# Kernel optimization log

Measured on AMD Instinct MI355X. Metric: run time of the kernel, lower is better.

Reference implementation:

```python
import jax, jax.numpy as jnp
import numpy as np

NOPEN = 64
NNIN = 16
NUM_OUTPUT = 64
NLAYER = 4
H = 0.1
TF = 1.0
N_NODES = 50000
N_EDGES = 1600000


def setup_inputs() -> dict:
    key = jax.random.key(0)
    k1, k2, k3, k4, k5, k6 = jax.random.split(key, 6)
    xn = jax.random.normal(k1, (1, NNIN, N_NODES), dtype=jnp.float32)
    iInd = jax.random.randint(k2, (N_EDGES,), 0, N_NODES)
    jInd = jax.random.randint(k3, (N_EDGES,), 0, N_NODES)
    # learned parameters per original init
    K1Nopen = jax.random.normal(k4, (NOPEN, NNIN), dtype=jnp.float32) * 0.01
    KN1 = jnp.eye(NOPEN, dtype=jnp.float32) + jax.random.uniform(k5, (NOPEN, NOPEN), dtype=jnp.float32) * 0.001
    KNclose = jax.random.normal(k6, (NUM_OUTPUT, NOPEN), dtype=jnp.float32) * 0.01
    return {"xn": xn, "iInd": iInd, "jInd": jInd, "n_nodes": N_NODES,
            "K1Nopen": K1Nopen, "KN1": KN1, "KNclose": KNclose}


def _gcn_norm(I, J, n_nodes, dtype):
    # add self-loops, symmetric normalization deg^{-1/2}[row]*deg^{-1/2}[col]
    loops = jnp.arange(n_nodes, dtype=I.dtype)
    I2 = jnp.concatenate([I, loops])
    J2 = jnp.concatenate([J, loops])
    ew = jnp.ones(I2.shape[0], dtype=dtype)
    deg = jax.ops.segment_sum(ew, J2, num_segments=n_nodes)
    dinv = jnp.where(deg > 0, 1.0 / jnp.sqrt(deg), 0.0)
    w = dinv[I2] * dinv[J2]
    return I2, J2, w


def reference(xn, iInd, jInd, n_nodes, K1Nopen, KN1, KNclose):
    I, J, w = _gcn_norm(iInd, jInd, n_nodes, xn.dtype)  # [E+N]

    # OpenFlatLayer: 1x1 conv1d with K1Nopen + relu (openclose=True, norm=False)
    x = jax.nn.relu(jnp.einsum('oi,bin->bon', K1Nopen, xn))  # [1, nopen, N]

    dt = TF / NLAYER
    wb = w[None, None, :]
    for _ in range(NLAYER):
        # nodeGrad: edge features [1, nopen, E]
        g = wb * (x[:, :, I] - x[:, :, J])
        # singleLayer (openclose=False): conv(K), relu, conv(K.t())
        z = jax.nn.relu(jnp.einsum('oi,bie->boe', KN1, g))
        z = jnp.einsum('io,bie->boe', KN1, z)
        # edgeDiv: scatter-add w*z at I minus at J
        wz = jnp.moveaxis(wb * z, -1, 0)  # [E, 1, nopen]
        div = (jax.ops.segment_sum(wz, I, num_segments=n_nodes)
               - jax.ops.segment_sum(wz, J, num_segments=n_nodes))
        div = jnp.moveaxis(div, 0, -1)  # [1, nopen, N]
        # forward Euler: step layer returns -h*div, integrated with dt
        x = x - dt * H * div

    # CloseLayer: 1x1 conv1d, squeeze().t(), log_softmax over channels
    xc = jnp.einsum('oi,bin->bon', KNclose, x)[0].T  # [N, num_output]
    return jax.nn.log_softmax(xc, axis=1)
```

## Files before the change

### kernel.cpp

```cpp
#include <hip/hip_runtime.h>

#define NN 50000
#define NE 1600000
#define C 64
#define NIN 16
#define DTH 0.025f
#define ASC 16.0f
#define USC 64.0f
#define SDIV 16384.0f
#define SLOT 128

#define NB2 256
#define NPB 196
#define CAP 16384
#define ABLK 1024
#define EPB 1563
#define RND 2048
#define BINC 32

typedef _Float16 f16x2 __attribute__((ext_vector_type(2)));
typedef float f32x2 __attribute__((ext_vector_type(2)));
union U32H2 { uint32_t u; f16x2 h; };

__global__ void k_setup(const float* __restrict__ KN1, const float* __restrict__ KNc,
                        const float* __restrict__ K1,
                        float* __restrict__ KN1T, float* __restrict__ KNcT,
                        float* __restrict__ K1T, float* __restrict__ M2s,
                        float* __restrict__ KMs, int* __restrict__ gcur) {
    if (threadIdx.x < NB2) gcur[threadIdx.x] = 0;
    for (int idx = threadIdx.x; idx < C * C; idx += blockDim.x) {
        int o = idx >> 6, i = idx & 63;
        KN1T[i * C + o] = KN1[o * C + i];
        KNcT[i * C + o] = KNc[o * C + i];
    }
    for (int idx = threadIdx.x; idx < C * NIN; idx += blockDim.x) {
        int o = idx >> 4, i = idx & 15;
        K1T[i * C + o] = K1[o * NIN + i];
    }
    for (int idx = threadIdx.x; idx < C * C; idx += blockDim.x) {
        int p = idx >> 6, o = idx & 63;
        float s1 = 0.f, s2 = 0.f;
        for (int i = 0; i < C; i++) {
            s1 = fmaf(KN1[o * C + i], KN1[p * C + i], s1);
            s2 = fmaf(KNc[o * C + i], KN1[p * C + i], s2);
        }
        M2s[idx] = s1;
        KMs[idx] = s2;
    }
}

__launch_bounds__(256)
__global__ void k_binA(const int* __restrict__ iInd, const int* __restrict__ jInd,
                       int* __restrict__ gcur, uint32_t* __restrict__ stg) {
    __shared__ uint32_t bins[NB2][BINC];
    __shared__ int bcnt[NB2];
    __shared__ int gbase[NB2];
    int tid = threadIdx.x;
    int eBeg = blockIdx.x * EPB;
    int eEnd = eBeg + EPB; if (eEnd > NE) eEnd = NE;
    for (int rb = eBeg; rb < eEnd; rb += RND) {
        for (int b = tid; b < NB2; b += 256) bcnt[b] = 0;
        __syncthreads();
        int rEnd = rb + RND; if (rEnd > eEnd) rEnd = eEnd;
        for (int e = rb + tid; e < rEnd; e += 256) {
            int i = __builtin_nontemporal_load(&iInd[e]);
            int j = __builtin_nontemporal_load(&jInd[e]);
            {
                int b = (unsigned)i / NPB;
                uint32_t ent = ((unsigned)(i - b * NPB) << 17) | (unsigned)j;
                int pos = atomicAdd(&bcnt[b], 1);
                if (pos < BINC) bins[b][pos] = ent;
                else { int gp = atomicAdd(&gcur[b], 1);
                       if (gp < CAP) stg[(size_t)b * CAP + gp] = ent; }
            }
            {
                int b = (unsigned)j / NPB;
                uint32_t ent = ((unsigned)(j - b * NPB) << 17) | 0x10000u | (unsigned)i;
                int pos = atomicAdd(&bcnt[b], 1);
                if (pos < BINC) bins[b][pos] = ent;
                else { int gp = atomicAdd(&gcur[b], 1);
                       if (gp < CAP) stg[(size_t)b * CAP + gp] = ent; }
            }
        }
        __syncthreads();
        {
            int c = bcnt[tid]; if (c > BINC) c = BINC;
            gbase[tid] = (c > 0) ? atomicAdd(&gcur[tid], c) : 0;
        }
        __syncthreads();
        for (int idx = tid; idx < NB2 * BINC; idx += 256) {
            int b = idx >> 5, k = idx & (BINC - 1);
            int c = bcnt[b]; if (c > BINC) c = BINC;
            if (k < c) {
                int pos = gbase[b] + k;
                if (pos < CAP) stg[(size_t)b * CAP + pos] = bins[b][k];
            }
        }
        __syncthreads();
    }
}

__launch_bounds__(1024)
__global__ void k_binB(const int* __restrict__ gcur, const uint32_t* __restrict__ stg,
                       unsigned* __restrict__ pk, float* __restrict__ dinv,
                       uint32_t* __restrict__ adjp) {
    __shared__ unsigned lcnt[NPB];
    int b = blockIdx.x, tid = threadIdx.x;
    if (tid < NPB) lcnt[tid] = 0;
    __syncthreads();
    int cnt = gcur[b]; if (cnt > CAP) cnt = CAP;
    int n0 = b * NPB;
    for (int k = tid; k < cnt; k += 1024) {
        uint32_t ent = stg[(size_t)b * CAP + k];
        int tl = (int)(ent >> 17);
        unsigned sign = (ent >> 16) & 1u;
        unsigned other = ent & 0xFFFFu;
        unsigned ret = atomicAdd(&lcnt[tl], 1u + (sign << 16));
        unsigned slot = ret & 0xFFFFu;
        if (slot < SLOT) adjp[(((unsigned)(n0 + tl)) << 7) + slot] = other | (sign << 31);
    }
    __syncthreads();
    if (tid < NPB) {
        int n = n0 + tid;
        if (n < NN) {
            unsigned v = lcnt[tid];
            unsigned c = v & 0xFFFFu; if (c > SLOT) c = SLOT;
            unsigned deg = (v >> 16) + 1u;
            pk[n] = (deg << 16) | c;
            dinv[n] = 1.0f / sqrtf((float)deg);
        }
    }
}

__global__ void k_weight(const unsigned* __restrict__ pk, const float* __restrict__ dinv,
                         uint32_t* __restrict__ adjp) {
    int idx = blockIdx.x * 256 + threadIdx.x;
    int n = idx >> 7, p = idx & (SLOT - 1);
    int cnt = (int)(pk[n] & 0xFFFFu); if (cnt > SLOT) cnt = SLOT;
    int pad = (cnt + 31) & ~31;
    if (p < cnt) {
        uint32_t e = adjp[idx];
        int other = (int)(e & 0xFFFFu);
        float a = ASC * dinv[n] * dinv[other];
        float w = 0.5f * a * a;
        if (e >> 31) w = -w;
        U32H2 t; t.u = (unsigned)other; t.h.y = (_Float16)w;
        adjp[idx] = t.u;
    } else if (p < pad) {
        adjp[idx] = 0u;
    }
}

static __device__ __forceinline__ void store_u8(uint32_t* __restrict__ u8, int n, int lane, float su) {
    float v1 = __shfl_down(su, 1, 64);
    float v2 = __shfl_down(su, 2, 64);
    float v3 = __shfl_down(su, 3, 64);
    if ((lane & 3) == 0) {
        int p0 = __builtin_amdgcn_cvt_pk_fp8_f32(su, v1, 0, false);
        int p1 = __builtin_amdgcn_cvt_pk_fp8_f32(v2, v3, p0, true);
        u8[n * 16 + (lane >> 2)] = (uint32_t)p1;
    }
}

__launch_bounds__(256)
__global__ void k_open_u(const float* __restrict__ xn, const float* __restrict__ K1T,
                         const float* __restrict__ KN1T, const float* __restrict__ KNcT,
                         _Float16* __restrict__ u0, uint32_t* __restrict__ u8,
                         float* __restrict__ co) {
    __shared__ float sK1T[NIN * C];
    __shared__ float sKT[C * C];
    __shared__ float sKc[C * C];
    for (int idx = threadIdx.x; idx < NIN * C; idx += 256) sK1T[idx] = K1T[idx];
    for (int idx = threadIdx.x; idx < C * C; idx += 256) { sKT[idx] = KN1T[idx]; sKc[idx] = KNcT[idx]; }
    __syncthreads();
    int wv = threadIdx.x >> 6, lane = threadIdx.x & 63;
    int n = blockIdx.x * 4 + wv;
    float acc = 0.f;
#pragma unroll
    for (int i = 0; i < NIN; i++)
        acc = fmaf(sK1T[i * C + lane], xn[i * NN + n], acc);
    float xr = fmaxf(acc, 0.f);
    float ua = 0.f, oc = 0.f;
    for (int i = 0; i < C; i++) {
        float xi = __shfl(xr, i, 64);
        ua = fmaf(sKT[i * C + lane], xi, ua);
        oc = fmaf(sKc[i * C + lane], xi, oc);
    }
    u0[(size_t)n * C + lane] = (_Float16)ua;
    store_u8(u8, n, lane, ua * USC);
    co[(size_t)n * C + lane] = oc;
}

#define ACCR(WW, QQ, A0, A1, A2, A3, U0, U1, U2, U3) {                        \
    U32H2 aw; aw.u = (WW);                                                    \
    float w_ = (float)aw.h.y;                                                 \
    f32x2 lo_ = __builtin_amdgcn_cvt_pk_f32_fp8((int)(QQ), false);            \
    f32x2 hi_ = __builtin_amdgcn_cvt_pk_f32_fp8((int)(QQ), true);             \
    float d0_ = (U0) - lo_.x, d1_ = (U1) - lo_.y;                             \
    float d2_ = (U2) - hi_.x, d3_ = (U3) - hi_.y;                             \
    A0 = fmaf(w_, __builtin_fabsf(d0_), fmaf(__builtin_fabsf(w_), d0_, A0));  \
    A1 = fmaf(w_, __builtin_fabsf(d1_), fmaf(__builtin_fabsf(w_), d1_, A1));  \
    A2 = fmaf(w_, __builtin_fabsf(d2_), fmaf(__builtin_fabsf(w_), d2_, A2));  \
    A3 = fmaf(w_, __builtin_fabsf(d3_), fmaf(__builtin_fabsf(w_), d3_, A3));  \
}

#define GATHER2_BODY(PKA, ADJP, U8R)                                          \
    uint32_t unqA = (U8R)[nA * 16 + li];                                      \
    uint32_t unqB = (U8R)[nB * 16 + li];                                      \
    f32x2 alo = __builtin_amdgcn_cvt_pk_f32_fp8((int)unqA, false);            \
    f32x2 ahi = __builtin_amdgcn_cvt_pk_f32_fp8((int)unqA, true);             \
    f32x2 blo = __builtin_amdgcn_cvt_pk_f32_fp8((int)unqB, false);            \
    f32x2 bhi = __builtin_amdgcn_cvt_pk_f32_fp8((int)unqB, true);             \
    float uA0 = alo.x, uA1 = alo.y, uA2 = ahi.x, uA3 = ahi.y;                 \
    float uB0 = blo.x, uB1 = blo.y, uB2 = bhi.x, uB3 = bhi.y;                 \
    uint2 pk2_ = *(const uint2*)&(PKA)[nA];                                   \
    int degA = (int)(pk2_.x & 0xFFFFu); if (degA > SLOT) degA = SLOT;         \
    int degB = (int)(pk2_.y & 0xFFFFu); if (degB > SLOT) degB = SLOT;         \
    int padA = (degA + 31) & ~31, padB = (degB + 31) & ~31;                   \
    int baseA = nA << 7, baseB = nB << 7;                                     \
    int maxPad = padA > padB ? padA : padB;                                   \
    float aA0 = 0.f, aA1 = 0.f, aA2 = 0.f, aA3 = 0.f;                         \
    float aB0 = 0.f, aB1 = 0.f, aB2 = 0.f, aB3 = 0.f;                         \
    for (int c0 = 0; c0 < maxPad; c0 += 32) {                                 \
        uint32_t wA[8], qA[8], wB[8], qB[8];                                  \
        bool dA = c0 < padA, dB = c0 < padB;                                  \
        if (dA) {                                                             \
            _Pragma("unroll")                                                 \
            for (int r = 0; r < 8; r++) wA[r] = (ADJP)[baseA + c0 + r * 4 + g]; \
        }                                                                     \
        if (dB) {                                                             \
            _Pragma("unroll")                                                 \
            for (int r = 0; r < 8; r++) wB[r] = (ADJP)[baseB + c0 + r * 4 + g]; \
        }                                                                     \
        if (dA) {                                                             \
            _Pragma("unroll")                                                 \
            for (int r = 0; r < 8; r++) qA[r] = (U8R)[(wA[r] & 0xFFFFu) * 16 + li]; \
        }                                                                     \
        if (dB) {                                                             \
            _Pragma("unroll")                                                 \
            for (int r = 0; r < 8; r++) qB[r] = (U8R)[(wB[r] & 0xFFFFu) * 16 + li]; \
        }                                                                     \
        if (dA) {                                                             \
            _Pragma("unroll")                                                 \
            for (int r = 0; r < 8; r++) ACCR(wA[r], qA[r], aA0, aA1, aA2, aA3, uA0, uA1, uA2, uA3) \
        }                                                                     \
        if (dB) {                                                             \
            _Pragma("unroll")                                                 \
            for (int r = 0; r < 8; r++) ACCR(wB[r], qB[r], aB0, aB1, aB2, aB3, uB0, uB1, uB2, uB3) \
        }                                                                     \
    }                                                                         \
    aA0 += __shfl_xor(aA0, 16, 64); aA0 += __shfl_xor(aA0, 32, 64);           \
    aA1 += __shfl_xor(aA1, 16, 64); aA1 += __shfl_xor(aA1, 32, 64);           \
    aA2 += __shfl_xor(aA2, 16, 64); aA2 += __shfl_xor(aA2, 32, 64);           \
    aA3 += __shfl_xor(aA3, 16, 64); aA3 += __shfl_xor(aA3, 32, 64);           \
    aB0 += __shfl_xor(aB0, 16, 64); aB0 += __shfl_xor(aB0, 32, 64);           \
    aB1 += __shfl_xor(aB1, 16, 64); aB1 += __shfl_xor(aB1, 32, 64);           \
    aB2 += __shfl_xor(aB2, 16, 64); aB2 += __shfl_xor(aB2, 32, 64);           \
    aB3 += __shfl_xor(aB3, 16, 64); aB3 += __shfl_xor(aB3, 32, 64);           \
    float rA0 = __shfl(aA0, lane >> 2, 64), rA1 = __shfl(aA1, lane >> 2, 64); \
    float rA2 = __shfl(aA2, lane >> 2, 64), rA3 = __shfl(aA3, lane >> 2, 64); \
    float rB0 = __shfl(aB0, lane >> 2, 64), rB1 = __shfl(aB1, lane >> 2, 64); \
    float rB2 = __shfl(aB2, lane >> 2, 64), rB3 = __shfl(aB3, lane >> 2, 64); \
    float sA_lane = (lane & 2) ? ((lane & 1) ? rA3 : rA2)                     \
                               : ((lane & 1) ? rA1 : rA0);                    \
    float sB_lane = (lane & 2) ? ((lane & 1) ? rB3 : rB2)                     \
                               : ((lane & 1) ? rB1 : rB0);

#define RL(x, l) __int_as_float(__builtin_amdgcn_readlane(__float_as_int(x), (l)))

#define STAGE_MT(SMT, SRC) {                                                  \
    for (int idx = threadIdx.x; idx < C * C; idx += 256) {                    \
        int p_ = idx >> 6, c_ = idx & 63;                                     \
        (SMT)[(c_ << 6) | (p_ ^ ((c_ & 7) << 2))] = (SRC)[idx];               \
    }                                                                         \
}

#define MATVEC2(SMT, SAV, SBV, DUA, DUB) {                                    \
    float mA0_ = 0.f, mA1_ = 0.f, mB0_ = 0.f, mB1_ = 0.f;                     \
    int mb_ = (lane << 6), lx_ = (lane & 7) << 2;                             \
    _Pragma("unroll")                                                         \
    for (int p0 = 0; p0 < 64; p0 += 4) {                                      \
        const float4 mv = *(const float4*)&(SMT)[mb_ + (p0 ^ lx_)];           \
        mA0_ = fmaf(mv.x, RL(SAV, p0 + 0), mA0_);                             \
        mA1_ = fmaf(mv.y, RL(SAV, p0 + 1), mA1_);                             \
        mA0_ = fmaf(mv.z, RL(SAV, p0 + 2), mA0_);                             \
        mA1_ = fmaf(mv.w, RL(SAV, p0 + 3), mA1_);                             \
        mB0_ = fmaf(mv.x, RL(SBV, p0 + 0), mB0_);                             \
        mB1_ = fmaf(mv.y, RL(SBV, p0 + 1), mB1_);                             \
        mB0_ = fmaf(mv.z, RL(SBV, p0 + 2), mB0_);                             \
        mB1_ = fmaf(mv.w, RL(SBV, p0 + 3), mB1_);                             \
    }                                                                         \
    DUA = mA0_ + mA1_; DUB = mB0_ + mB1_;                                     \
}

__launch_bounds__(256, 8)
__global__ void k_gather_upd(const unsigned* __restrict__ pk, const uint32_t* __restrict__ adjp,
                             const uint32_t* __restrict__ u8r, const _Float16* __restrict__ ucur,
                             const float* __restrict__ M2s, float* __restrict__ sacc,
                             _Float16* __restrict__ unext, uint32_t* __restrict__ u8w, int beta) {
    __shared__ float sMt[C * C];
    STAGE_MT(sMt, M2s)
    __syncthreads();
    int wv = threadIdx.x >> 6, lane = threadIdx.x & 63;
    int g = lane >> 4, li = lane & 15;
    int nA = (blockIdx.x * 4 + wv) * 2;
    int nB = nA + 1;
    GATHER2_BODY(pk, adjp, u8r)
    float duA, duB;
    MATVEC2(sMt, sA_lane, sB_lane, duA, duB)
    float unewA = (float)ucur[(size_t)nA * C + lane] - (DTH / SDIV) * duA;
    float unewB = (float)ucur[(size_t)nB * C + lane] - (DTH / SDIV) * duB;
    unext[(size_t)nA * C + lane] = (_Float16)unewA;
    unext[(size_t)nB * C + lane] = (_Float16)unewB;
    store_u8(u8w, nA, lane, unewA * USC);
    store_u8(u8w, nB, lane, unewB * USC);
    size_t ixA = (size_t)nA * C + lane, ixB = (size_t)nB * C + lane;
    sacc[ixA] = beta ? (sacc[ixA] + sA_lane) : sA_lane;
    sacc[ixB] = beta ? (sacc[ixB] + sB_lane) : sB_lane;
}

__launch_bounds__(256, 8)
__global__ void k_gather_close(const unsigned* __restrict__ pk, const uint32_t* __restrict__ adjp,
                               const uint32_t* __restrict__ u8r, const float* __restrict__ KMs,
                               const float* __restrict__ sacc, const float* __restrict__ co,
                               float* __restrict__ out) {
    __shared__ float sKMt[C * C];
    STAGE_MT(sKMt, KMs)
    __syncthreads();
    int wv = threadIdx.x >> 6, lane = threadIdx.x & 63;
    int g = lane >> 4, li = lane & 15;
    int nA = (blockIdx.x * 4 + wv) * 2;
    int nB = nA + 1;
    GATHER2_BODY(pk, adjp, u8r)
    float stotA = sA_lane + sacc[(size_t)nA * C + lane];
    float stotB = sB_lane + sacc[(size_t)nB * C + lane];
    float dxA, dxB;
    MATVEC2(sKMt, stotA, stotB, dxA, dxB)
    float oA = co[(size_t)nA * C + lane] - (DTH / SDIV) * dxA;
    float oB = co[(size_t)nB * C + lane] - (DTH / SDIV) * dxB;
    float mA = oA, mB = oB;
#pragma unroll
    for (int off2 = 32; off2; off2 >>= 1) {
        mA = fmaxf(mA, __shfl_xor(mA, off2, 64));
        mB = fmaxf(mB, __shfl_xor(mB, off2, 64));
    }
    float sumA = expf(oA - mA), sumB = expf(oB - mB);
#pragma unroll
    for (int off2 = 32; off2; off2 >>= 1) {
        sumA += __shfl_xor(sumA, off2, 64);
        sumB += __shfl_xor(sumB, off2, 64);
    }
    out[(size_t)nA * C + lane] = oA - mA - logf(sumA);
    out[(size_t)nB * C + lane] = oB - mB - logf(sumB);
}

extern "C" void kernel_launch(void* const* d_in, const int* in_sizes, int n_in,
                              void* d_out, int out_size, void* d_ws, size_t ws_size,
                              hipStream_t stream) {
    (void)in_sizes; (void)n_in; (void)out_size; (void)ws_size;
    const float* xn   = (const float*)d_in[0];
    const int* iInd   = (const int*)d_in[1];
    const int* jInd   = (const int*)d_in[2];
    const float* K1   = (const float*)d_in[4];
    const float* KN1  = (const float*)d_in[5];
    const float* KNc  = (const float*)d_in[6];
    float* out = (float*)d_out;

    char* base = (char*)d_ws;
    size_t off = 0;
    auto alloc = [&](size_t bytes) { char* p = base + off; off = (off + bytes + 255) & ~(size_t)255; return p; };
    float* KN1T = (float*)alloc(C * C * 4);
    float* KNcT = (float*)alloc(C * C * 4);
    float* K1T  = (float*)alloc(NIN * C * 4);
    float* M2s  = (float*)alloc(C * C * 4);
    float* KMs  = (float*)alloc(C * C * 4);
    int* gcur   = (int*)alloc(NB2 * 4);
    unsigned* pk = (unsigned*)alloc(NN * 4);
    float* dinv = (float*)alloc(NN * 4);
    float* co   = (float*)alloc((size_t)NN * C * 4);
    float* sacc = (float*)alloc((size_t)NN * C * 4);
    _Float16* ua = (_Float16*)alloc((size_t)NN * C * 2);
    _Float16* ub = (_Float16*)alloc((size_t)NN * C * 2);
    uint32_t* u8a = (uint32_t*)alloc((size_t)NN * 16 * 4);
    uint32_t* u8b = (uint32_t*)alloc((size_t)NN * 16 * 4);
    uint32_t* stg = (uint32_t*)alloc((size_t)NB2 * CAP * 4);
    uint32_t* adjp = (uint32_t*)alloc((size_t)NN * SLOT * 4);

    k_setup<<<1, 256, 0, stream>>>(KN1, KNc, K1, KN1T, KNcT, K1T, M2s, KMs, gcur);
    k_binA<<<ABLK, 256, 0, stream>>>(iInd, jInd, gcur, stg);
    k_binB<<<NB2, 1024, 0, stream>>>(gcur, stg, pk, dinv, adjp);
    k_weight<<<(NN * SLOT) / 256, 256, 0, stream>>>(pk, dinv, adjp);

    k_open_u<<<NN / 4, 256, 0, stream>>>(xn, K1T, KN1T, KNcT, ua, u8a, co);

    const int GB = NN / 8;
    k_gather_upd<<<GB, 256, 0, stream>>>(pk, adjp, u8a, ua, M2s, sacc, ub, u8b, 0);
    k_gather_upd<<<GB, 256, 0, stream>>>(pk, adjp, u8b, ub, M2s, sacc, ua, u8a, 1);
    k_gather_upd<<<GB, 256, 0, stream>>>(pk, adjp, u8a, ua, M2s, sacc, ub, u8b, 1);
    k_gather_close<<<GB, 256, 0, stream>>>(pk, adjp, u8b, KMs, sacc, co, out);
}
```

Before: 520.1 us.

## Pad bin counters, stage adjacency in LDS, and restructure open kernel

The global bin counters are spread to one every 16 ints so that atomics on different bins no longer share a cache line. k_binB scatters adjacency slots into a 100KB LDS buffer and then writes them out with coalesced uint4 stores, replacing scattered global writes. k_open_u becomes a grid-stride persistent kernel with 512 threads. Each wave processes two nodes, reading weights from swizzled LDS as float4 and broadcasting activations with readlane instead of shfl, which removes the separate transposes in k_setup. The large LDS allocation limits k_binB occupancy, and the LDS copy writes unused padding slots to global memory.

Result: faster. 508.2 us (-2.3%).

```diff
diff --git a/kernel.cpp b/kernel.cpp
--- a/kernel.cpp
+++ b/kernel.cpp
@@ -17,26 +17,19 @@
 #define EPB 1563
 #define RND 2048
 #define BINC 32
+#define GSTR 16
+#define OPEN_GRID 1024
 
 typedef _Float16 f16x2 __attribute__((ext_vector_type(2)));
 typedef float f32x2 __attribute__((ext_vector_type(2)));
 union U32H2 { uint32_t u; f16x2 h; };
 
+#define RL(x, l) __int_as_float(__builtin_amdgcn_readlane(__float_as_int(x), (l)))
+
 __global__ void k_setup(const float* __restrict__ KN1, const float* __restrict__ KNc,
-                        const float* __restrict__ K1,
-                        float* __restrict__ KN1T, float* __restrict__ KNcT,
-                        float* __restrict__ K1T, float* __restrict__ M2s,
-                        float* __restrict__ KMs, int* __restrict__ gcur) {
-    if (threadIdx.x < NB2) gcur[threadIdx.x] = 0;
-    for (int idx = threadIdx.x; idx < C * C; idx += blockDim.x) {
-        int o = idx >> 6, i = idx & 63;
-        KN1T[i * C + o] = KN1[o * C + i];
-        KNcT[i * C + o] = KNc[o * C + i];
-    }
-    for (int idx = threadIdx.x; idx < C * NIN; idx += blockDim.x) {
-        int o = idx >> 4, i = idx & 15;
-        K1T[i * C + o] = K1[o * NIN + i];
-    }
+                        float* __restrict__ M2s, float* __restrict__ KMs,
+                        int* __restrict__ gcur) {
+    if (threadIdx.x < NB2) gcur[threadIdx.x * GSTR] = 0;
     for (int idx = threadIdx.x; idx < C * C; idx += blockDim.x) {
         int p = idx >> 6, o = idx & 63;
         float s1 = 0.f, s2 = 0.f;
@@ -70,7 +63,7 @@
                 uint32_t ent = ((unsigned)(i - b * NPB) << 17) | (unsigned)j;
                 int pos = atomicAdd(&bcnt[b], 1);
                 if (pos < BINC) bins[b][pos] = ent;
-                else { int gp = atomicAdd(&gcur[b], 1);
+                else { int gp = atomicAdd(&gcur[b * GSTR], 1);
                        if (gp < CAP) stg[(size_t)b * CAP + gp] = ent; }
             }
             {
@@ -78,14 +71,14 @@
                 uint32_t ent = ((unsigned)(j - b * NPB) << 17) | 0x10000u | (unsigned)i;
                 int pos = atomicAdd(&bcnt[b], 1);
                 if (pos < BINC) bins[b][pos] = ent;
-                else { int gp = atomicAdd(&gcur[b], 1);
+                else { int gp = atomicAdd(&gcur[b * GSTR], 1);
                        if (gp < CAP) stg[(size_t)b * CAP + gp] = ent; }
             }
         }
         __syncthreads();
         {
             int c = bcnt[tid]; if (c > BINC) c = BINC;
-            gbase[tid] = (c > 0) ? atomicAdd(&gcur[tid], c) : 0;
+            gbase[tid] = (c > 0) ? atomicAdd(&gcur[tid * GSTR], c) : 0;
         }
         __syncthreads();
         for (int idx = tid; idx < NB2 * BINC; idx += 256) {
@@ -100,15 +93,17 @@
     }
 }
 
+#define LADJ (NPB * SLOT)
 __launch_bounds__(1024)
 __global__ void k_binB(const int* __restrict__ gcur, const uint32_t* __restrict__ stg,
                        unsigned* __restrict__ pk, float* __restrict__ dinv,
                        uint32_t* __restrict__ adjp) {
     __shared__ unsigned lcnt[NPB];
+    __shared__ uint32_t ladj[LADJ];
     int b = blockIdx.x, tid = threadIdx.x;
     if (tid < NPB) lcnt[tid] = 0;
     __syncthreads();
-    int cnt = gcur[b]; if (cnt > CAP) cnt = CAP;
+    int cnt = gcur[b * GSTR]; if (cnt > CAP) cnt = CAP;
     int n0 = b * NPB;
     for (int k = tid; k < cnt; k += 1024) {
         uint32_t ent = stg[(size_t)b * CAP + k];
@@ -117,7 +112,7 @@
         unsigned other = ent & 0xFFFFu;
         unsigned ret = atomicAdd(&lcnt[tl], 1u + (sign << 16));
         unsigned slot = ret & 0xFFFFu;
-        if (slot < SLOT) adjp[(((unsigned)(n0 + tl)) << 7) + slot] = other | (sign << 31);
+        if (slot < SLOT) ladj[(tl << 7) + slot] = other | (sign << 31);
     }
     __syncthreads();
     if (tid < NPB) {
@@ -130,6 +125,11 @@
             dinv[n] = 1.0f / sqrtf((float)deg);
         }
     }
+    int nval = NN - n0; if (nval > NPB) nval = NPB; if (nval < 0) nval = 0;
+    int totv = (nval << 7) >> 2;
+    uint4* gdst = (uint4*)(adjp + ((size_t)n0 << 7));
+    const uint4* lsrc = (const uint4*)ladj;
+    for (int v = tid; v < totv; v += 1024) gdst[v] = lsrc[v];
 }
 
 __global__ void k_weight(const unsigned* __restrict__ pk, const float* __restrict__ dinv,
@@ -162,33 +162,64 @@
     }
 }
 
-__launch_bounds__(256)
-__global__ void k_open_u(const float* __restrict__ xn, const float* __restrict__ K1T,
-                         const float* __restrict__ KN1T, const float* __restrict__ KNcT,
+__launch_bounds__(512)
+__global__ void k_open_u(const float* __restrict__ xn, const float* __restrict__ K1,
+                         const float* __restrict__ KN1, const float* __restrict__ KNc,
                          _Float16* __restrict__ u0, uint32_t* __restrict__ u8,
                          float* __restrict__ co) {
-    __shared__ float sK1T[NIN * C];
-    __shared__ float sKT[C * C];
-    __shared__ float sKc[C * C];
-    for (int idx = threadIdx.x; idx < NIN * C; idx += 256) sK1T[idx] = K1T[idx];
-    for (int idx = threadIdx.x; idx < C * C; idx += 256) { sKT[idx] = KN1T[idx]; sKc[idx] = KNcT[idx]; }
+    __shared__ float sK1[NIN * C];
+    __shared__ float sU[C * C];
+    __shared__ float sC[C * C];
+    for (int idx = threadIdx.x; idx < NIN * C; idx += 512) {
+        int i = idx >> 6, o = idx & 63;
+        sK1[idx] = K1[o * NIN + i];
+    }
+    for (int idx = threadIdx.x; idx < C * C; idx += 512) {
+        int o = idx >> 6, p = idx & 63;
+        int sw = (o << 6) | (p ^ ((o & 7) << 2));
+        sU[sw] = KN1[idx];
+        sC[sw] = KNc[idx];
+    }
     __syncthreads();
     int wv = threadIdx.x >> 6, lane = threadIdx.x & 63;
-    int n = blockIdx.x * 4 + wv;
-    float acc = 0.f;
+    int mb = lane << 6, lx = (lane & 7) << 2;
+    for (int pr = blockIdx.x * 8 + wv; pr < NN / 2; pr += OPEN_GRID * 8) {
+        int nA = pr * 2, nB = nA + 1;
+        float xA = 0.f, xB = 0.f;
 #pragma unroll
-    for (int i = 0; i < NIN; i++)
-        acc = fmaf(sK1T[i * C + lane], xn[i * NN + n], acc);
-    float xr = fmaxf(acc, 0.f);
-    float ua = 0.f, oc = 0.f;
-    for (int i = 0; i < C; i++) {
-        float xi = __shfl(xr, i, 64);
-        ua = fmaf(sKT[i * C + lane], xi, ua);
-        oc = fmaf(sKc[i * C + lane], xi, oc);
-    }
-    u0[(size_t)n * C + lane] = (_Float16)ua;
-    store_u8(u8, n, lane, ua * USC);
-    co[(size_t)n * C + lane] = oc;
+        for (int i = 0; i < NIN; i++) {
+            float k1 = sK1[i * C + lane];
+            xA = fmaf(k1, xn[i * NN + nA], xA);
+            xB = fmaf(k1, xn[i * NN + nB], xB);
+        }
+        xA = fmaxf(xA, 0.f); xB = fmaxf(xB, 0.f);
+        float uA0 = 0.f, uA1 = 0.f, uB0 = 0.f, uB1 = 0.f;
+        float cA0 = 0.f, cA1 = 0.f, cB0 = 0.f, cB1 = 0.f;
+#pragma unroll
+        for (int p0 = 0; p0 < C; p0 += 4) {
+            const float4 mu = *(const float4*)&sU[mb + (p0 ^ lx)];
+            const float4 mc = *(const float4*)&sC[mb + (p0 ^ lx)];
+            float a0 = RL(xA, p0 + 0), a1 = RL(xA, p0 + 1);
+            float a2 = RL(xA, p0 + 2), a3 = RL(xA, p0 + 3);
+            float b0 = RL(xB, p0 + 0), b1 = RL(xB, p0 + 1);
+            float b2 = RL(xB, p0 + 2), b3 = RL(xB, p0 + 3);
+            uA0 = fmaf(mu.x, a0, uA0); uA1 = fmaf(mu.y, a1, uA1);
+            uA0 = fmaf(mu.z, a2, uA0); uA1 = fmaf(mu.w, a3, uA1);
+            uB0 = fmaf(mu.x, b0, uB0); uB1 = fmaf(mu.y, b1, uB1);
+            uB0 = fmaf(mu.z, b2, uB0); uB1 = fmaf(mu.w, b3, uB1);
+            cA0 = fmaf(mc.x, a0, cA0); cA1 = fmaf(mc.y, a1, cA1);
+            cA0 = fmaf(mc.z, a2, cA0); cA1 = fmaf(mc.w, a3, cA1);
+            cB0 = fmaf(mc.x, b0, cB0); cB1 = fmaf(mc.y, b1, cB1);
+            cB0 = fmaf(mc.z, b2, cB0); cB1 = fmaf(mc.w, b3, cB1);
+        }
+        float uA = uA0 + uA1, uB = uB0 + uB1;
+        u0[(size_t)nA * C + lane] = (_Float16)uA;
+        u0[(size_t)nB * C + lane] = (_Float16)uB;
+        store_u8(u8, nA, lane, uA * USC);
+        store_u8(u8, nB, lane, uB * USC);
+        co[(size_t)nA * C + lane] = cA0 + cA1;
+        co[(size_t)nB * C + lane] = cB0 + cB1;
+    }
 }
 
 #define ACCR(WW, QQ, A0, A1, A2, A3, U0, U1, U2, U3) {                        \
@@ -265,8 +296,6 @@
                                : ((lane & 1) ? rA1 : rA0);                    \
     float sB_lane = (lane & 2) ? ((lane & 1) ? rB3 : rB2)                     \
                                : ((lane & 1) ? rB1 : rB0);
-
-#define RL(x, l) __int_as_float(__builtin_amdgcn_readlane(__float_as_int(x), (l)))
 
 #define STAGE_MT(SMT, SRC) {                                                  \
     for (int idx = threadIdx.x; idx < C * C; idx += 256) {                    \
@@ -369,12 +398,9 @@
     char* base = (char*)d_ws;
     size_t off = 0;
     auto alloc = [&](size_t bytes) { char* p = base + off; off = (off + bytes + 255) & ~(size_t)255; return p; };
-    float* KN1T = (float*)alloc(C * C * 4);
-    float* KNcT = (float*)alloc(C * C * 4);
-    float* K1T  = (float*)alloc(NIN * C * 4);
     float* M2s  = (float*)alloc(C * C * 4);
     float* KMs  = (float*)alloc(C * C * 4);
-    int* gcur   = (int*)alloc(NB2 * 4);
+    int* gcur   = (int*)alloc(NB2 * GSTR * 4);
     unsigned* pk = (unsigned*)alloc(NN * 4);
     float* dinv = (float*)alloc(NN * 4);
     float* co   = (float*)alloc((size_t)NN * C * 4);
@@ -386,12 +412,12 @@
     uint32_t* stg = (uint32_t*)alloc((size_t)NB2 * CAP * 4);
     uint32_t* adjp = (uint32_t*)alloc((size_t)NN * SLOT * 4);
 
-    k_setup<<<1, 256, 0, stream>>>(KN1, KNc, K1, KN1T, KNcT, K1T, M2s, KMs, gcur);
+    k_setup<<<1, 256, 0, stream>>>(KN1, KNc, M2s, KMs, gcur);
     k_binA<<<ABLK, 256, 0, stream>>>(iInd, jInd, gcur, stg);
     k_binB<<<NB2, 1024, 0, stream>>>(gcur, stg, pk, dinv, adjp);
     k_weight<<<(NN * SLOT) / 256, 256, 0, stream>>>(pk, dinv, adjp);
 
-    k_open_u<<<NN / 4, 256, 0, stream>>>(xn, K1T, KN1T, KNcT, ua, u8a, co);
+    k_open_u<<<OPEN_GRID, 512, 0, stream>>>(xn, K1, KN1, KNc, ua, u8a, co);
 
     const int GB = NN / 8;
     k_gather_upd<<<GB, 256, 0, stream>>>(pk, adjp, u8a, ua, M2s, sacc, ub, u8b, 0);
```
